# Optimization experiments

Measured on AMD Instinct MI355X. Metric: run time of the kernel, lower is better.

## Reference

```python
import jax, jax.numpy as jnp
import numpy as np

N = 50000       # nodes
E = 800000      # directed edges (before self-loops)
IN_C = 128
HID = 32
HEADS = 4
OUT_C = 64
NEG_SLOPE = 0.2  # PyG GATConv default leaky relu slope


def setup_inputs() -> dict:
    key = jax.random.key(0)
    ks = jax.random.split(key, 11)
    x = jax.random.normal(ks[0], (N, IN_C), jnp.float32)
    edge_index = jax.random.randint(ks[1], (2, E), 0, N, dtype=jnp.int32)
    # conv1: in -> HEADS*HID, concat=True
    W1 = jax.random.normal(ks[2], (IN_C, HEADS * HID), jnp.float32) / np.sqrt(IN_C)
    att_src1 = jax.random.normal(ks[3], (HEADS, HID), jnp.float32) / np.sqrt(HID)
    att_dst1 = jax.random.normal(ks[4], (HEADS, HID), jnp.float32) / np.sqrt(HID)
    b1 = jnp.zeros((HEADS * HID,), jnp.float32)
    # conv2: HEADS*HID -> OUT_C, heads=1, concat=False
    W2 = jax.random.normal(ks[5], (HEADS * HID, OUT_C), jnp.float32) / np.sqrt(HEADS * HID)
    att_src2 = jax.random.normal(ks[6], (1, OUT_C), jnp.float32) / np.sqrt(OUT_C)
    att_dst2 = jax.random.normal(ks[7], (1, OUT_C), jnp.float32) / np.sqrt(OUT_C)
    b2 = jnp.zeros((OUT_C,), jnp.float32)
    return dict(x=x, edge_index=edge_index, W1=W1, att_src1=att_src1,
                att_dst1=att_dst1, b1=b1, W2=W2, att_src2=att_src2,
                att_dst2=att_dst2, b2=b2)


def _gat_conv(x, src, dst, W, att_src, att_dst, bias, heads, ch, concat):
    # x: [N, F_in]; src/dst: [E'] (self-loops already included)
    h = (x @ W).reshape(N, heads, ch)                 # [N, H, C]
    a_s = jnp.sum(h * att_src[None], axis=-1)         # [N, H]
    a_d = jnp.sum(h * att_dst[None], axis=-1)         # [N, H]
    e = jax.nn.leaky_relu(a_s[src] + a_d[dst], NEG_SLOPE)  # [E', H]
    # numerically-stable edge softmax over destination neighborhoods
    m = jax.ops.segment_max(e, dst, num_segments=N)   # [N, H]
    m = jnp.where(jnp.isfinite(m), m, 0.0)
    ee = jnp.exp(e - jax.lax.stop_gradient(m)[dst])
    denom = jax.ops.segment_sum(ee, dst, num_segments=N)  # [N, H]
    alpha = ee / (denom[dst] + 1e-16)                 # [E', H]
    msg = h[src] * alpha[:, :, None]                  # [E', H, C]
    out = jax.ops.segment_sum(msg, dst, num_segments=N)   # [N, H, C]
    if concat:
        out = out.reshape(N, heads * ch)
    else:
        out = out.mean(axis=1)
    return out + bias


def reference(x, edge_index, W1, att_src1, att_dst1, b1, W2, att_src2, att_dst2, b2):
    # PyG GATConv adds self-loops by default
    loop = jnp.arange(N, dtype=edge_index.dtype)
    src = jnp.concatenate([edge_index[0], loop])
    dst = jnp.concatenate([edge_index[1], loop])
    # dropout layers are identity in eval mode (training=False)
    h = _gat_conv(x, src, dst, W1, att_src1, att_dst1, b1, HEADS, HID, True)
    h = jax.nn.elu(h)
    out = _gat_conv(h, src, dst, W2, att_src2, att_dst2, b2, 1, OUT_C, False)
    return out
```

## Files before the change

kernel.cpp:

```cpp
#include <hip/hip_runtime.h>
#include <math.h>

namespace {
constexpr int N_   = 50000;
constexpr int E_   = 800000;
constexpr int EP_  = E_ + N_;
constexpr float SLOPE = 0.2f;

constexpr int NB_    = (N_ + 127) / 128;
constexpr int CHUNK_ = 8192;
constexpr int NBLKA_ = (EP_ + CHUNK_ - 1) / CHUNK_;
constexpr int CAPB_  = 4096;
constexpr int NBLKG_ = (N_ + 63) / 64;

constexpr size_t OFF_H1  = 0;
constexpr size_t OFF_Y1  = OFF_H1  + (size_t)N_ * 128 * 2;
constexpr size_t OFF_H2  = OFF_Y1  + (size_t)N_ * 128 * 2;
constexpr size_t OFF_AS1 = OFF_H2  + (size_t)N_ * 64 * 2;
constexpr size_t OFF_AD1 = OFF_AS1 + (size_t)N_ * 4 * 4;
constexpr size_t OFF_AS2 = OFF_AD1 + (size_t)N_ * 4 * 4;
constexpr size_t OFF_AD2 = OFF_AS2 + (size_t)N_ * 4;
constexpr size_t OFF_ROW = OFF_AD2 + (size_t)N_ * 4;
constexpr size_t OFF_GC  = OFF_ROW + (((size_t)(N_ + 1) * 4 + 15) & ~(size_t)15);
constexpr size_t OFF_GO  = OFF_GC  + (((size_t)NB_ * 4 + 15) & ~(size_t)15);
constexpr size_t OFF_GU  = OFF_GO  + (((size_t)(NB_ + 1) * 4 + 15) & ~(size_t)15);
constexpr size_t OFF_EB1 = OFF_GU  + (((size_t)NB_ * 4 + 15) & ~(size_t)15);
constexpr size_t OFF_EB  = OFF_EB1 + (size_t)EP_ * 4;
}

typedef __attribute__((ext_vector_type(8))) short short8;
typedef __attribute__((ext_vector_type(4))) float f32x4;

__device__ __forceinline__ unsigned short f2bf(float x) {
  unsigned u = __float_as_uint(x);
  return (unsigned short)((u + 0x7FFFu + ((u >> 16) & 1u)) >> 16);
}
__device__ __forceinline__ unsigned pack2bf(float a, float b) {
  return (unsigned)f2bf(a) | ((unsigned)f2bf(b) << 16);
}
__device__ __forceinline__ float bf_lo(unsigned u) { return __uint_as_float(u << 16); }
__device__ __forceinline__ float bf_hi(unsigned u) { return __uint_as_float(u & 0xFFFF0000u); }

__global__ __launch_bounds__(256, 3) void k_gemm1(const float* __restrict__ x,
    const float* __restrict__ W, const float* __restrict__ av_s,
    const float* __restrict__ av_d, unsigned short* __restrict__ hbf,
    float* __restrict__ a_s, float* __restrict__ a_d)
{
  __shared__ __align__(16) char smem[52224];
  unsigned short* xs = (unsigned short*)smem;
  unsigned*       wt = (unsigned*)(smem + 17408);
  float*         wtf = (float*)(smem + 17408);
  const int t = threadIdx.x;
  const int rbase = blockIdx.x * 64;
#pragma unroll
  for (int it = 0; it < 8; ++it) {
    const int fidx = t + it * 256;
    const int row = fidx >> 5;
    const int c4  = fidx & 31;
    const int rg  = rbase + row;
    float4 v = (rg < N_) ? ((const float4*)x)[(size_t)rg * 32 + c4]
                         : make_float4(0.f, 0.f, 0.f, 0.f);
    *(uint2*)&xs[row * 136 + c4 * 4] =
        make_uint2(pack2bf(v.x, v.y), pack2bf(v.z, v.w));
  }
#pragma unroll
  for (int it = 0; it < 32; ++it) {
    const int idx = t + it * 256;
    const int n  = idx & 127;
    const int kk = idx >> 7;
    wt[n * 68 + kk] = pack2bf(W[(2 * kk) * 128 + n], W[(2 * kk + 1) * 128 + n]);
  }
  __syncthreads();
  const int wv = t >> 6;
  const int l  = t & 63;
  const int lr = l & 15;
  const int lg = l >> 4;
  f32x4 acc[8];
#pragma unroll
  for (int j = 0; j < 8; ++j) acc[j] = (f32x4){0.f, 0.f, 0.f, 0.f};
#pragma unroll
  for (int ks = 0; ks < 4; ++ks) {
    const short8 a = *(const short8*)&xs[(wv * 16 + lr) * 136 + ks * 32 + lg * 8];
#pragma unroll
    for (int j = 0; j < 8; ++j) {
      const short8 b = *(const short8*)&wt[(j * 16 + lr) * 68 + ks * 16 + lg * 4];
      acc[j] = __builtin_amdgcn_mfma_f32_16x16x32_bf16(a, b, acc[j], 0, 0, 0);
    }
  }
  __syncthreads();
#pragma unroll
  for (int j = 0; j < 8; ++j)
#pragma unroll
    for (int r = 0; r < 4; ++r)
      wtf[(wv * 16 + lg * 4 + r) * 132 + j * 16 + lr] = acc[j][r];
  __syncthreads();
#pragma unroll
  for (int it = 0; it < 16; ++it) {
    const int idx = t + it * 256;
    const int row = idx >> 6;
    const int c2  = idx & 63;
    const int rg  = rbase + row;
    if (rg < N_) {
      const float2 hv = *(const float2*)&wtf[row * 132 + c2 * 2];
      ((unsigned*)hbf)[(size_t)rg * 64 + c2] = pack2bf(hv.x, hv.y);
    }
  }
  {
    const int row = t & 63;
    const int q   = t >> 6;
    const int rg  = rbase + row;
    float ss = 0.f, sd = 0.f;
#pragma unroll
    for (int i = 0; i < 8; ++i) {
      const float4 hv = *(const float4*)&wtf[row * 132 + q * 32 + 4 * i];
      const float4 s4 = *(const float4*)&av_s[q * 32 + 4 * i];
      const float4 d4 = *(const float4*)&av_d[q * 32 + 4 * i];
      ss += hv.x * s4.x + hv.y * s4.y + hv.z * s4.z + hv.w * s4.w;
      sd += hv.x * d4.x + hv.y * d4.y + hv.z * d4.z + hv.w * d4.w;
    }
    if (rg < N_) { a_s[rg * 4 + q] = ss; a_d[rg * 4 + q] = sd; }
  }
}

__global__ __launch_bounds__(256, 4) void k_gemm2(const unsigned* __restrict__ ybf,
    const float* __restrict__ W, const float* __restrict__ av_s,
    const float* __restrict__ av_d, unsigned short* __restrict__ hbf,
    float* __restrict__ a_s, float* __restrict__ a_d)
{
  __shared__ __align__(16) char smem[36864];
  unsigned short* xs = (unsigned short*)smem;
  unsigned*       wt = (unsigned*)(smem + 17408);
  float*         wtf = (float*)(smem + 17408);
  float*          ps = (float*)(smem + 34816);
  const int t = threadIdx.x;
  const int rbase = blockIdx.x * 64;
#pragma unroll
  for (int it = 0; it < 16; ++it) {
    const int idx = t + it * 256;
    const int row = idx >> 6;
    const int c2  = idx & 63;
    const int rg  = rbase + row;
    const unsigned u = (rg < N_) ? ybf[(size_t)rg * 64 + c2] : 0u;
    *(unsigned*)&xs[row * 136 + c2 * 2] = u;
  }
#pragma unroll
  for (int it = 0; it < 16; ++it) {
    const int idx = t + it * 256;
    const int n  = idx & 63;
    const int kk = idx >> 6;
    wt[n * 68 + kk] = pack2bf(W[(2 * kk) * 64 + n], W[(2 * kk + 1) * 64 + n]);
  }
  __syncthreads();
  const int wv = t >> 6;
  const int l  = t & 63;
  const int lr = l & 15;
  const int lg = l >> 4;
  f32x4 acc[4];
#pragma unroll
  for (int j = 0; j < 4; ++j) acc[j] = (f32x4){0.f, 0.f, 0.f, 0.f};
#pragma unroll
  for (int ks = 0; ks < 4; ++ks) {
    const short8 a = *(const short8*)&xs[(wv * 16 + lr) * 136 + ks * 32 + lg * 8];
#pragma unroll
    for (int j = 0; j < 4; ++j) {
      const short8 b = *(const short8*)&wt[(j * 16 + lr) * 68 + ks * 16 + lg * 4];
      acc[j] = __builtin_amdgcn_mfma_f32_16x16x32_bf16(a, b, acc[j], 0, 0, 0);
    }
  }
  __syncthreads();
#pragma unroll
  for (int j = 0; j < 4; ++j)
#pragma unroll
    for (int r = 0; r < 4; ++r)
      wtf[(wv * 16 + lg * 4 + r) * 68 + j * 16 + lr] = acc[j][r];
  __syncthreads();
#pragma unroll
  for (int it = 0; it < 8; ++it) {
    const int idx = t + it * 256;
    const int row = idx >> 5;
    const int c2  = idx & 31;
    const int rg  = rbase + row;
    if (rg < N_) {
      const float2 hv = *(const float2*)&wtf[row * 68 + c2 * 2];
      ((unsigned*)hbf)[(size_t)rg * 32 + c2] = pack2bf(hv.x, hv.y);
    }
  }
  {
    const int row = t & 63;
    const int g   = t >> 6;
    float ss = 0.f, sd = 0.f;
#pragma unroll
    for (int i = 0; i < 4; ++i) {
      const float4 hv = *(const float4*)&wtf[row * 68 + g * 16 + 4 * i];
      const float4 s4 = *(const float4*)&av_s[g * 16 + 4 * i];
      const float4 d4 = *(const float4*)&av_d[g * 16 + 4 * i];
      ss += hv.x * s4.x + hv.y * s4.y + hv.z * s4.z + hv.w * s4.w;
      sd += hv.x * d4.x + hv.y * d4.y + hv.z * d4.z + hv.w * d4.w;
    }
    ps[g * 64 + row] = ss;
    ps[256 + g * 64 + row] = sd;
  }
  __syncthreads();
  if (t < 64) {
    const int rg = rbase + t;
    if (rg < N_) {
      a_s[rg] = ps[t] + ps[64 + t] + ps[128 + t] + ps[192 + t];
      a_d[rg] = ps[256 + t] + ps[320 + t] + ps[384 + t] + ps[448 + t];
    }
  }
}

__global__ __launch_bounds__(256) void k_hist(const int* __restrict__ ei,
                                              int* __restrict__ gcount)
{
  __shared__ int nh[NB_];
  const int t = threadIdx.x;
  for (int j = t; j < NB_; j += 256) nh[j] = 0;
  __syncthreads();
  const int beg = blockIdx.x * CHUNK_;
  const int end = min(beg + CHUNK_, EP_);
  for (int i = beg + t; i < end; i += 256) {
    const int d = (i < E_) ? ei[E_ + i] : (i - E_);
    atomicAdd(&nh[d >> 7], 1);
  }
  __syncthreads();
  for (int j = t; j < NB_; j += 256)
    if (nh[j]) atomicAdd(&gcount[j], nh[j]);
}

__global__ __launch_bounds__(512) void k_scan(const int* __restrict__ gcount,
    int* __restrict__ goff, int* __restrict__ gcursor)
{
  __shared__ int sd[512];
  const int t = threadIdx.x;
  const int v = (t < NB_) ? gcount[t] : 0;
  sd[t] = v;
  __syncthreads();
  for (int off = 1; off < 512; off <<= 1) {
    const int add = (t >= off) ? sd[t - off] : 0;
    __syncthreads();
    sd[t] += add;
    __syncthreads();
  }
  if (t < NB_) { goff[t] = sd[t] - v; gcursor[t] = sd[t] - v; }
  if (t == 0) goff[NB_] = EP_;
}

__global__ __launch_bounds__(256) void k_scatter(const int* __restrict__ ei,
    int* __restrict__ gcursor, unsigned* __restrict__ eb1)
{
  __shared__ int nh[NB_];
  __shared__ int gb[NB_];
  const int t = threadIdx.x;
  for (int j = t; j < NB_; j += 256) nh[j] = 0;
  __syncthreads();
  const int beg = blockIdx.x * CHUNK_;
  const int end = min(beg + CHUNK_, EP_);
  for (int i = beg + t; i < end; i += 256) {
    const int d = (i < E_) ? ei[E_ + i] : (i - E_);
    atomicAdd(&nh[d >> 7], 1);
  }
  __syncthreads();
  for (int j = t; j < NB_; j += 256) {
    const int c = nh[j];
    gb[j] = c ? atomicAdd(&gcursor[j], c) : 0;
    nh[j] = 0;
  }
  __syncthreads();
  for (int i = beg + t; i < end; i += 256) {
    int s, d;
    if (i < E_) { s = ei[i]; d = ei[E_ + i]; } else { s = d = i - E_; }
    const int b = d >> 7;
    const int r = atomicAdd(&nh[b], 1);
    eb1[gb[b] + r] = ((unsigned)s << 16) | (unsigned)d;
  }
}

__global__ __launch_bounds__(256) void k_bucket(const unsigned* __restrict__ eb1,
    const int* __restrict__ goff, int* __restrict__ rowptr,
    int* __restrict__ ebuf)
{
  __shared__ int h[128];
  __shared__ int off[129];
  __shared__ unsigned arrv[CAPB_];
  const int b = blockIdx.x;
  const int t = threadIdx.x;
  const int base = goff[b];
  const int cnt  = goff[b + 1] - base;
  if (t < 128) h[t] = 0;
  __syncthreads();
  const bool fits = (cnt <= CAPB_);
  for (int i = t; i < cnt; i += 256) {
    const unsigned v = eb1[base + i];
    if (fits) arrv[i] = v;
    atomicAdd(&h[(int)(v & 0xFFFFu) - (b << 7)], 1);
  }
  __syncthreads();
  if (t < 64) {
    const int a0 = h[2 * t], a1 = h[2 * t + 1];
    int s = a0 + a1;
#pragma unroll
    for (int m = 1; m < 64; m <<= 1) {
      const int u = __shfl_up(s, m);
      if (t >= m) s += u;
    }
    off[2 * t + 1] = s - a1;
    off[2 * t]     = s - a1 - a0;
    if (t == 63) off[128] = s;
  }
  __syncthreads();
  if (t < 128) {
    const int dst = (b << 7) + t;
    if (dst < N_) rowptr[dst] = base + off[t];
  }
  if (b == NB_ - 1 && t == 0) rowptr[N_] = EP_;
  if (t < 128) h[t] = 0;
  __syncthreads();
  for (int i = t; i < cnt; i += 256) {
    const unsigned v = fits ? arrv[i] : eb1[base + i];
    const int dlow = (int)(v & 0xFFFFu) - (b << 7);
    const int r = atomicAdd(&h[dlow], 1);
    ebuf[base + off[dlow] + r] = (int)(v >> 16);
  }
}

__global__ __launch_bounds__(256, 4) void k_agg1(const int* __restrict__ rowptr,
    const int* __restrict__ ebuf, const float* __restrict__ a_s,
    const float* __restrict__ a_d, const unsigned short* __restrict__ hbf,
    const float* __restrict__ b1, unsigned* __restrict__ y)
{
  __shared__ uint2 pl[4][4 * 65];
  const int w = threadIdx.x >> 6;
  const int l = threadIdx.x & 63;
  const int d = blockIdx.x * 4 + w;
  const int base = rowptr[d];
  const int deg  = rowptr[d + 1] - base;
  const float4 ad = *(const float4*)&a_d[(size_t)d * 4];
  const int hsel = l >> 4;
  const unsigned l4 = (unsigned)l * 4u;
  float acc0 = 0.f, acc1 = 0.f;
  float r0, r1, r2, r3;

  if (deg <= 64) {
    int   sreg = 0;
    float e0 = -1e30f, e1 = -1e30f, e2 = -1e30f, e3 = -1e30f;
    if (l < deg) {
      sreg = ebuf[base + l];
      const float4 as = *(const float4*)&a_s[(size_t)sreg * 4];
      e0 = as.x + ad.x; e0 = e0 > 0.f ? e0 : SLOPE * e0;
      e1 = as.y + ad.y; e1 = e1 > 0.f ? e1 : SLOPE * e1;
      e2 = as.z + ad.z; e2 = e2 > 0.f ? e2 : SLOPE * e2;
      e3 = as.w + ad.w; e3 = e3 > 0.f ? e3 : SLOPE * e3;
    }
    float mx0 = e0, mx1 = e1, mx2 = e2, mx3 = e3;
#pragma unroll
    for (int m = 32; m >= 1; m >>= 1) {
      mx0 = fmaxf(mx0, __shfl_xor(mx0, m));
      mx1 = fmaxf(mx1, __shfl_xor(mx1, m));
      mx2 = fmaxf(mx2, __shfl_xor(mx2, m));
      mx3 = fmaxf(mx3, __shfl_xor(mx3, m));
    }
    const float p0 = (l < deg) ? __expf(e0 - mx0) : 0.f;
    const float p1 = (l < deg) ? __expf(e1 - mx1) : 0.f;
    const float p2 = (l < deg) ? __expf(e2 - mx2) : 0.f;
    const float p3 = (l < deg) ? __expf(e3 - mx3) : 0.f;
    float sm0 = p0, sm1 = p1, sm2 = p2, sm3 = p3;
#pragma unroll
    for (int m = 32; m >= 1; m >>= 1) {
      sm0 += __shfl_xor(sm0, m);
      sm1 += __shfl_xor(sm1, m);
      sm2 += __shfl_xor(sm2, m);
      sm3 += __shfl_xor(sm3, m);
    }
    r0 = 1.f / (sm0 + 1e-16f);
    r1 = 1.f / (sm1 + 1e-16f);
    r2 = 1.f / (sm2 + 1e-16f);
    r3 = 1.f / (sm3 + 1e-16f);
    {
      const unsigned soff = (unsigned)sreg << 8;
      pl[w][0 * 65 + l] = make_uint2(soff, __float_as_uint(p0));
      pl[w][1 * 65 + l] = make_uint2(soff, __float_as_uint(p1));
      pl[w][2 * 65 + l] = make_uint2(soff, __float_as_uint(p2));
      pl[w][3 * 65 + l] = make_uint2(soff, __float_as_uint(p3));
    }
    const uint2* __restrict__ rp = &pl[w][hsel * 65];
    const int niter = (deg + 7) >> 3;
    int it = 0;
    for (; it + 2 <= niter; it += 2) {
      unsigned uA[8], uB[8];
      float pA[8], pB[8];
#pragma unroll
      for (int u = 0; u < 8; ++u) {
        const uint2 sp = rp[it * 8 + u];
        pA[u] = __uint_as_float(sp.y);
        uA[u] = *(const unsigned*)((const char*)hbf + (sp.x + l4));
      }
#pragma unroll
      for (int u = 0; u < 8; ++u) {
        const uint2 sp = rp[it * 8 + 8 + u];
        pB[u] = __uint_as_float(sp.y);
        uB[u] = *(const unsigned*)((const char*)hbf + (sp.x + l4));
      }
#pragma unroll
      for (int u = 0; u < 8; ++u) {
        acc0 = fmaf(pA[u], bf_lo(uA[u]), acc0);
        acc1 = fmaf(pA[u], bf_hi(uA[u]), acc1);
      }
#pragma unroll
      for (int u = 0; u < 8; ++u) {
        acc0 = fmaf(pB[u], bf_lo(uB[u]), acc0);
        acc1 = fmaf(pB[u], bf_hi(uB[u]), acc1);
      }
    }
    if (it < niter) {
      unsigned uA[8];
      float pA[8];
#pragma unroll
      for (int u = 0; u < 8; ++u) {
        const uint2 sp = rp[it * 8 + u];
        pA[u] = __uint_as_float(sp.y);
        uA[u] = *(const unsigned*)((const char*)hbf + (sp.x + l4));
      }
#pragma unroll
      for (int u = 0; u < 8; ++u) {
        acc0 = fmaf(pA[u], bf_lo(uA[u]), acc0);
        acc1 = fmaf(pA[u], bf_hi(uA[u]), acc1);
      }
    }
  } else {
    float mx0 = -1e30f, mx1 = -1e30f, mx2 = -1e30f, mx3 = -1e30f;
    for (int i = l; i < deg; i += 64) {
      const int s = ebuf[base + i];
      const float4 as = *(const float4*)&a_s[(size_t)s * 4];
      float e0 = as.x + ad.x; e0 = e0 > 0.f ? e0 : SLOPE * e0;
      float e1 = as.y + ad.y; e1 = e1 > 0.f ? e1 : SLOPE * e1;
      float e2 = as.z + ad.z; e2 = e2 > 0.f ? e2 : SLOPE * e2;
      float e3 = as.w + ad.w; e3 = e3 > 0.f ? e3 : SLOPE * e3;
      mx0 = fmaxf(mx0, e0); mx1 = fmaxf(mx1, e1);
      mx2 = fmaxf(mx2, e2); mx3 = fmaxf(mx3, e3);
    }
#pragma unroll
    for (int m = 32; m >= 1; m >>= 1) {
      mx0 = fmaxf(mx0, __shfl_xor(mx0, m));
      mx1 = fmaxf(mx1, __shfl_xor(mx1, m));
      mx2 = fmaxf(mx2, __shfl_xor(mx2, m));
      mx3 = fmaxf(mx3, __shfl_xor(mx3, m));
    }
    float sm0 = 0.f, sm1 = 0.f, sm2 = 0.f, sm3 = 0.f;
    for (int i = l; i < deg; i += 64) {
      const int s = ebuf[base + i];
      const float4 as = *(const float4*)&a_s[(size_t)s * 4];
      float e0 = as.x + ad.x; e0 = e0 > 0.f ? e0 : SLOPE * e0;
      float e1 = as.y + ad.y; e1 = e1 > 0.f ? e1 : SLOPE * e1;
      float e2 = as.z + ad.z; e2 = e2 > 0.f ? e2 : SLOPE * e2;
      float e3 = as.w + ad.w; e3 = e3 > 0.f ? e3 : SLOPE * e3;
      sm0 += __expf(e0 - mx0); sm1 += __expf(e1 - mx1);
      sm2 += __expf(e2 - mx2); sm3 += __expf(e3 - mx3);
    }
#pragma unroll
    for (int m = 32; m >= 1; m >>= 1) {
      sm0 += __shfl_xor(sm0, m);
      sm1 += __shfl_xor(sm1, m);
      sm2 += __shfl_xor(sm2, m);
      sm3 += __shfl_xor(sm3, m);
    }
    r0 = 1.f / (sm0 + 1e-16f);
    r1 = 1.f / (sm1 + 1e-16f);
    r2 = 1.f / (sm2 + 1e-16f);
    r3 = 1.f / (sm3 + 1e-16f);
    const float mxs = hsel == 3 ? mx3 : hsel == 2 ? mx2 : hsel == 1 ? mx1 : mx0;
    for (int i = 0; i < deg; ++i) {
      const int s = ebuf[base + i];
      const float4 as = *(const float4*)&a_s[(size_t)s * 4];
      float e0 = as.x + ad.x; e0 = e0 > 0.f ? e0 : SLOPE * e0;
      float e1 = as.y + ad.y; e1 = e1 > 0.f ? e1 : SLOPE * e1;
      float e2 = as.z + ad.z; e2 = e2 > 0.f ? e2 : SLOPE * e2;
      float e3 = as.w + ad.w; e3 = e3 > 0.f ? e3 : SLOPE * e3;
      const float es = hsel == 3 ? e3 : hsel == 2 ? e2 : hsel == 1 ? e1 : e0;
      const float pa = __expf(es - mxs);
      const unsigned uu = ((const unsigned*)(hbf + (size_t)s * 128))[l];
      acc0 = fmaf(pa, bf_lo(uu), acc0);
      acc1 = fmaf(pa, bf_hi(uu), acc1);
    }
  }
  const float rsel = hsel == 3 ? r3 : hsel == 2 ? r2 : hsel == 1 ? r1 : r0;
  const int c0 = 2 * l;
  const float2 bb = *(const float2*)&b1[c0];
  float o0 = acc0 * rsel + bb.x;
  float o1 = acc1 * rsel + bb.y;
  o0 = o0 > 0.f ? o0 : expm1f(o0);
  o1 = o1 > 0.f ? o1 : expm1f(o1);
  y[(size_t)d * 64 + l] = pack2bf(o0, o1);
}

__global__ __launch_bounds__(256, 4) void k_agg2(const int* __restrict__ rowptr,
    const int* __restrict__ ebuf, const float* __restrict__ a_s,
    const float* __restrict__ a_d, const unsigned short* __restrict__ hbf,
    const float* __restrict__ b2, float* __restrict__ out)
{
  __shared__ uint2 pl2[4][66];
  const int w = threadIdx.x >> 6;
  const int l = threadIdx.x & 63;
  const int lh = l & 31;
  const bool hi = (l >= 32);
  const int d = blockIdx.x * 4 + w;
  const int base = rowptr[d];
  const int deg  = rowptr[d + 1] - base;
  const float ad = a_d[d];
  const unsigned lh4 = (unsigned)lh * 4u;
  float acc0 = 0.f, acc1 = 0.f;
  float rv;

  if (deg <= 64) {
    int   sreg = 0;
    float e = -1e30f;
    if (l < deg) {
      sreg = ebuf[base + l];
      e = a_s[sreg] + ad; e = e > 0.f ? e : SLOPE * e;
    }
    float mx = e;
#pragma unroll
    for (int m = 32; m >= 1; m >>= 1) mx = fmaxf(mx, __shfl_xor(mx, m));
    const float p = (l < deg) ? __expf(e - mx) : 0.f;
    float sm = p;
#pragma unroll
    for (int m = 32; m >= 1; m >>= 1) sm += __shfl_xor(sm, m);
    rv = 1.f / (sm + 1e-16f);
    pl2[w][l] = make_uint2((unsigned)(l < deg ? sreg : 0) << 7,
                           __float_as_uint(p));
    const uint2* __restrict__ rp = &pl2[w][hi ? 1 : 0];
    const int niter = (deg + 15) >> 4;
    int it = 0;
    for (; it + 2 <= niter; it += 2) {
      unsigned uA[8], uB[8];
      float pA[8], pB[8];
#pragma unroll
      for (int u = 0; u < 8; ++u) {
        const uint2 sp = rp[it * 16 + 2 * u];
        pA[u] = __uint_as_float(sp.y);
        uA[u] = *(const unsigned*)((const char*)hbf + (sp.x + lh4));
      }
#pragma unroll
      for (int u = 0; u < 8; ++u) {
        const uint2 sp = rp[it * 16 + 16 + 2 * u];
        pB[u] = __uint_as_float(sp.y);
        uB[u] = *(const unsigned*)((const char*)hbf + (sp.x + lh4));
      }
#pragma unroll
      for (int u = 0; u < 8; ++u) {
        acc0 = fmaf(pA[u], bf_lo(uA[u]), acc0);
        acc1 = fmaf(pA[u], bf_hi(uA[u]), acc1);
      }
#pragma unroll
      for (int u = 0; u < 8; ++u) {
        acc0 = fmaf(pB[u], bf_lo(uB[u]), acc0);
        acc1 = fmaf(pB[u], bf_hi(uB[u]), acc1);
      }
    }
    if (it < niter) {
      unsigned uA[8];
      float pA[8];
#pragma unroll
      for (int u = 0; u < 8; ++u) {
        const uint2 sp = rp[it * 16 + 2 * u];
        pA[u] = __uint_as_float(sp.y);
        uA[u] = *(const unsigned*)((const char*)hbf + (sp.x + lh4));
      }
#pragma unroll
      for (int u = 0; u < 8; ++u) {
        acc0 = fmaf(pA[u], bf_lo(uA[u]), acc0);
        acc1 = fmaf(pA[u], bf_hi(uA[u]), acc1);
      }
    }
  } else {
    float mx = -1e30f;
    for (int i = l; i < deg; i += 64) {
      const int s = ebuf[base + i];
      float e = a_s[s] + ad; e = e > 0.f ? e : SLOPE * e;
      mx = fmaxf(mx, e);
    }
#pragma unroll
    for (int m = 32; m >= 1; m >>= 1) mx = fmaxf(mx, __shfl_xor(mx, m));
    float sm = 0.f;
    for (int i = l; i < deg; i += 64) {
      const int s = ebuf[base + i];
      float e = a_s[s] + ad; e = e > 0.f ? e : SLOPE * e;
      sm += __expf(e - mx);
    }
#pragma unroll
    for (int m = 32; m >= 1; m >>= 1) sm += __shfl_xor(sm, m);
    rv = 1.f / (sm + 1e-16f);
    for (int i = 0; i < deg; ++i) {
      const int s = ebuf[base + i];
      float e = a_s[s] + ad; e = e > 0.f ? e : SLOPE * e;
      const float pp = hi ? 0.f : __expf(e - mx);
      const unsigned uu = ((const unsigned*)(hbf + (size_t)s * 64))[lh];
      acc0 = fmaf(pp, bf_lo(uu), acc0);
      acc1 = fmaf(pp, bf_hi(uu), acc1);
    }
  }
  acc0 += __shfl_xor(acc0, 32);
  acc1 += __shfl_xor(acc1, 32);
  if (!hi) {
    const int c0 = 2 * lh;
    const float2 bb = *(const float2*)&b2[c0];
    *(float2*)&out[(size_t)d * 64 + c0] =
        make_float2(acc0 * rv + bb.x, acc1 * rv + bb.y);
  }
}

extern "C" void kernel_launch(void* const* d_in, const int* in_sizes, int n_in,
                              void* d_out, int out_size, void* d_ws, size_t ws_size,
                              hipStream_t stream) {
  const float* x     = (const float*)d_in[0];
  const int*   ei    = (const int*)d_in[1];
  const float* W1    = (const float*)d_in[2];
  const float* as1v  = (const float*)d_in[3];
  const float* ad1v  = (const float*)d_in[4];
  const float* b1    = (const float*)d_in[5];
  const float* W2    = (const float*)d_in[6];
  const float* as2v  = (const float*)d_in[7];
  const float* ad2v  = (const float*)d_in[8];
  const float* b2    = (const float*)d_in[9];
  float* out = (float*)d_out;

  char* ws = (char*)d_ws;
  unsigned short* h1 = (unsigned short*)(ws + OFF_H1);
  unsigned* y1       = (unsigned*)(ws + OFF_Y1);
  unsigned short* h2 = (unsigned short*)(ws + OFF_H2);
  float* a_s1 = (float*)(ws + OFF_AS1);
  float* a_d1 = (float*)(ws + OFF_AD1);
  float* a_s2 = (float*)(ws + OFF_AS2);
  float* a_d2 = (float*)(ws + OFF_AD2);
  int* rowptr = (int*)(ws + OFF_ROW);
  int* gcount = (int*)(ws + OFF_GC);
  int* goff   = (int*)(ws + OFF_GO);
  int* gcur   = (int*)(ws + OFF_GU);
  unsigned* eb1 = (unsigned*)(ws + OFF_EB1);
  int* ebuf   = (int*)(ws + OFF_EB);

  hipMemsetAsync(gcount, 0, (size_t)NB_ * 4, stream);

  k_gemm1<<<NBLKG_, 256, 0, stream>>>(x, W1, as1v, ad1v, h1, a_s1, a_d1);
  k_hist<<<NBLKA_, 256, 0, stream>>>(ei, gcount);
  k_scan<<<1, 512, 0, stream>>>(gcount, goff, gcur);
  k_scatter<<<NBLKA_, 256, 0, stream>>>(ei, gcur, eb1);
  k_bucket<<<NB_, 256, 0, stream>>>(eb1, goff, rowptr, ebuf);
  k_agg1<<<N_ / 4, 256, 0, stream>>>(rowptr, ebuf, a_s1, a_d1, h1, b1, y1);
  k_gemm2<<<NBLKG_, 256, 0, stream>>>(y1, W2, as2v, ad2v, h2, a_s2, a_d2);
  k_agg2<<<N_ / 4, 256, 0, stream>>>(rowptr, ebuf, a_s2, a_d2, h2, b2, out);
}
```

Measured before the change: 149.8 us.

## Split agg1 nodes across two waves and fold histogram into gemm1 launch

The layer-1 aggregation now assigns two waves to each destination node. Each wave covers half of the channels, and the two half-waves of a wave process alternating edges; the partial sums are combined with a cross-half shuffle. This shortens the serial edge loop per wave and doubles the grid size. In exchange, the edge-softmax statistics are computed redundantly by both waves. Separately, the degree-histogram kernel is merged into the gemm1 launch as extra blocks, removing one launch and letting the two run concurrently.

After: 178.9 us. +19.4%, slower.

```diff
diff --git a/kernel.cpp b/kernel.cpp
--- a/kernel.cpp
+++ b/kernel.cpp
@@ -41,16 +41,32 @@
 __device__ __forceinline__ float bf_lo(unsigned u) { return __uint_as_float(u << 16); }
 __device__ __forceinline__ float bf_hi(unsigned u) { return __uint_as_float(u & 0xFFFF0000u); }
 
-__global__ __launch_bounds__(256, 3) void k_gemm1(const float* __restrict__ x,
+__global__ __launch_bounds__(256, 3) void k_g1h(const float* __restrict__ x,
     const float* __restrict__ W, const float* __restrict__ av_s,
     const float* __restrict__ av_d, unsigned short* __restrict__ hbf,
-    float* __restrict__ a_s, float* __restrict__ a_d)
+    float* __restrict__ a_s, float* __restrict__ a_d,
+    const int* __restrict__ ei, int* __restrict__ gcount)
 {
   __shared__ __align__(16) char smem[52224];
+  const int t = threadIdx.x;
+  if (blockIdx.x >= NBLKG_) {
+    int* nh = (int*)smem;
+    for (int j = t; j < NB_; j += 256) nh[j] = 0;
+    __syncthreads();
+    const int beg = (blockIdx.x - NBLKG_) * CHUNK_;
+    const int end = min(beg + CHUNK_, EP_);
+    for (int i = beg + t; i < end; i += 256) {
+      const int dd = (i < E_) ? ei[E_ + i] : (i - E_);
+      atomicAdd(&nh[dd >> 7], 1);
+    }
+    __syncthreads();
+    for (int j = t; j < NB_; j += 256)
+      if (nh[j]) atomicAdd(&gcount[j], nh[j]);
+    return;
+  }
   unsigned short* xs = (unsigned short*)smem;
   unsigned*       wt = (unsigned*)(smem + 17408);
   float*         wtf = (float*)(smem + 17408);
-  const int t = threadIdx.x;
   const int rbase = blockIdx.x * 64;
 #pragma unroll
   for (int it = 0; it < 8; ++it) {
@@ -210,24 +226,6 @@
   }
 }
 
-__global__ __launch_bounds__(256) void k_hist(const int* __restrict__ ei,
-                                              int* __restrict__ gcount)
-{
-  __shared__ int nh[NB_];
-  const int t = threadIdx.x;
-  for (int j = t; j < NB_; j += 256) nh[j] = 0;
-  __syncthreads();
-  const int beg = blockIdx.x * CHUNK_;
-  const int end = min(beg + CHUNK_, EP_);
-  for (int i = beg + t; i < end; i += 256) {
-    const int d = (i < E_) ? ei[E_ + i] : (i - E_);
-    atomicAdd(&nh[d >> 7], 1);
-  }
-  __syncthreads();
-  for (int j = t; j < NB_; j += 256)
-    if (nh[j]) atomicAdd(&gcount[j], nh[j]);
-}
-
 __global__ __launch_bounds__(512) void k_scan(const int* __restrict__ gcount,
     int* __restrict__ goff, int* __restrict__ gcursor)
 {
@@ -332,12 +330,15 @@
   __shared__ uint2 pl[4][4 * 65];
   const int w = threadIdx.x >> 6;
   const int l = threadIdx.x & 63;
-  const int d = blockIdx.x * 4 + w;
+  const int d = blockIdx.x * 2 + (w >> 1);
+  const int half = w & 1;
   const int base = rowptr[d];
   const int deg  = rowptr[d + 1] - base;
   const float4 ad = *(const float4*)&a_d[(size_t)d * 4];
-  const int hsel = l >> 4;
-  const unsigned l4 = (unsigned)l * 4u;
+  const int pe = l >> 5;
+  const int ci = half * 32 + (l & 31);
+  const int hsel = ci >> 4;
+  const unsigned ci4 = (unsigned)ci * 4u;
   float acc0 = 0.f, acc1 = 0.f;
   float r0, r1, r2, r3;
 
@@ -383,23 +384,23 @@
       pl[w][2 * 65 + l] = make_uint2(soff, __float_as_uint(p2));
       pl[w][3 * 65 + l] = make_uint2(soff, __float_as_uint(p3));
     }
-    const uint2* __restrict__ rp = &pl[w][hsel * 65];
-    const int niter = (deg + 7) >> 3;
+    const uint2* __restrict__ rp = &pl[w][hsel * 65 + pe];
+    const int niter = (deg + 15) >> 4;
     int it = 0;
     for (; it + 2 <= niter; it += 2) {
       unsigned uA[8], uB[8];
       float pA[8], pB[8];
 #pragma unroll
       for (int u = 0; u < 8; ++u) {
-        const uint2 sp = rp[it * 8 + u];
+        const uint2 sp = rp[it * 16 + 2 * u];
         pA[u] = __uint_as_float(sp.y);
-        uA[u] = *(const unsigned*)((const char*)hbf + (sp.x + l4));
-      }
-#pragma unroll
-      for (int u = 0; u < 8; ++u) {
-        const uint2 sp = rp[it * 8 + 8 + u];
+        uA[u] = *(const unsigned*)((const char*)hbf + (sp.x + ci4));
+      }
+#pragma unroll
+      for (int u = 0; u < 8; ++u) {
+        const uint2 sp = rp[it * 16 + 16 + 2 * u];
         pB[u] = __uint_as_float(sp.y);
-        uB[u] = *(const unsigned*)((const char*)hbf + (sp.x + l4));
+        uB[u] = *(const unsigned*)((const char*)hbf + (sp.x + ci4));
       }
 #pragma unroll
       for (int u = 0; u < 8; ++u) {
@@ -417,9 +418,9 @@
       float pA[8];
 #pragma unroll
       for (int u = 0; u < 8; ++u) {
-        const uint2 sp = rp[it * 8 + u];
+        const uint2 sp = rp[it * 16 + 2 * u];
         pA[u] = __uint_as_float(sp.y);
-        uA[u] = *(const unsigned*)((const char*)hbf + (sp.x + l4));
+        uA[u] = *(const unsigned*)((const char*)hbf + (sp.x + ci4));
       }
 #pragma unroll
       for (int u = 0; u < 8; ++u) {
@@ -469,28 +470,35 @@
     r2 = 1.f / (sm2 + 1e-16f);
     r3 = 1.f / (sm3 + 1e-16f);
     const float mxs = hsel == 3 ? mx3 : hsel == 2 ? mx2 : hsel == 1 ? mx1 : mx0;
-    for (int i = 0; i < deg; ++i) {
-      const int s = ebuf[base + i];
-      const float4 as = *(const float4*)&a_s[(size_t)s * 4];
-      float e0 = as.x + ad.x; e0 = e0 > 0.f ? e0 : SLOPE * e0;
-      float e1 = as.y + ad.y; e1 = e1 > 0.f ? e1 : SLOPE * e1;
-      float e2 = as.z + ad.z; e2 = e2 > 0.f ? e2 : SLOPE * e2;
-      float e3 = as.w + ad.w; e3 = e3 > 0.f ? e3 : SLOPE * e3;
-      const float es = hsel == 3 ? e3 : hsel == 2 ? e2 : hsel == 1 ? e1 : e0;
-      const float pa = __expf(es - mxs);
-      const unsigned uu = ((const unsigned*)(hbf + (size_t)s * 128))[l];
-      acc0 = fmaf(pa, bf_lo(uu), acc0);
-      acc1 = fmaf(pa, bf_hi(uu), acc1);
-    }
-  }
-  const float rsel = hsel == 3 ? r3 : hsel == 2 ? r2 : hsel == 1 ? r1 : r0;
-  const int c0 = 2 * l;
-  const float2 bb = *(const float2*)&b1[c0];
-  float o0 = acc0 * rsel + bb.x;
-  float o1 = acc1 * rsel + bb.y;
-  o0 = o0 > 0.f ? o0 : expm1f(o0);
-  o1 = o1 > 0.f ? o1 : expm1f(o1);
-  y[(size_t)d * 64 + l] = pack2bf(o0, o1);
+    for (int i = 0; i < deg; i += 2) {
+      const int e = i + pe;
+      if (e < deg) {
+        const int s = ebuf[base + e];
+        const float4 as = *(const float4*)&a_s[(size_t)s * 4];
+        float e0 = as.x + ad.x; e0 = e0 > 0.f ? e0 : SLOPE * e0;
+        float e1 = as.y + ad.y; e1 = e1 > 0.f ? e1 : SLOPE * e1;
+        float e2 = as.z + ad.z; e2 = e2 > 0.f ? e2 : SLOPE * e2;
+        float e3 = as.w + ad.w; e3 = e3 > 0.f ? e3 : SLOPE * e3;
+        const float es = hsel == 3 ? e3 : hsel == 2 ? e2 : hsel == 1 ? e1 : e0;
+        const float pa = __expf(es - mxs);
+        const unsigned uu = ((const unsigned*)(hbf + (size_t)s * 128))[ci];
+        acc0 = fmaf(pa, bf_lo(uu), acc0);
+        acc1 = fmaf(pa, bf_hi(uu), acc1);
+      }
+    }
+  }
+  acc0 += __shfl_xor(acc0, 32);
+  acc1 += __shfl_xor(acc1, 32);
+  if (pe == 0) {
+    const float rsel = hsel == 3 ? r3 : hsel == 2 ? r2 : hsel == 1 ? r1 : r0;
+    const int c0 = 2 * ci;
+    const float2 bb = *(const float2*)&b1[c0];
+    float o0 = acc0 * rsel + bb.x;
+    float o1 = acc1 * rsel + bb.y;
+    o0 = o0 > 0.f ? o0 : expm1f(o0);
+    o1 = o1 > 0.f ? o1 : expm1f(o1);
+    y[(size_t)d * 64 + ci] = pack2bf(o0, o1);
+  }
 }
 
 __global__ __launch_bounds__(256, 4) void k_agg2(const int* __restrict__ rowptr,
@@ -641,12 +649,12 @@
 
   hipMemsetAsync(gcount, 0, (size_t)NB_ * 4, stream);
 
-  k_gemm1<<<NBLKG_, 256, 0, stream>>>(x, W1, as1v, ad1v, h1, a_s1, a_d1);
-  k_hist<<<NBLKA_, 256, 0, stream>>>(ei, gcount);
+  k_g1h<<<NBLKG_ + NBLKA_, 256, 0, stream>>>(x, W1, as1v, ad1v, h1, a_s1, a_d1,
+                                             ei, gcount);
   k_scan<<<1, 512, 0, stream>>>(gcount, goff, gcur);
   k_scatter<<<NBLKA_, 256, 0, stream>>>(ei, gcur, eb1);
   k_bucket<<<NB_, 256, 0, stream>>>(eb1, goff, rowptr, ebuf);
-  k_agg1<<<N_ / 4, 256, 0, stream>>>(rowptr, ebuf, a_s1, a_d1, h1, b1, y1);
+  k_agg1<<<N_ / 2, 256, 0, stream>>>(rowptr, ebuf, a_s1, a_d1, h1, b1, y1);
   k_gemm2<<<NBLKG_, 256, 0, stream>>>(y1, W2, as2v, ad2v, h2, a_s2, a_d2);
   k_agg2<<<N_ / 4, 256, 0, stream>>>(rowptr, ebuf, a_s2, a_d2, h2, b2, out);
 }
```

## Fuse histogram into gemm1 launch and sort agg1 edges by source chunk

Applied to the files above, without the earlier changes.

The destination histogram kernel is merged into the first GEMM kernel as extra blocks, removing one launch and letting the histogram run alongside the GEMM. In the layer-1 aggregation, each wave sorts its edge list in shared memory by a coarse source-index bucket (sreg>>13) using ballots and popcounts, so that gathers of h rows from nearby sources are grouped for better cache locality. This adds eight ballots and some ALU work per node. The GEMM blocks now share their launch with lighter histogram blocks.

Measured after the change: 147.7 us. About the same (-1.4%).

```diff
diff --git a/kernel.cpp b/kernel.cpp
--- a/kernel.cpp
+++ b/kernel.cpp
@@ -41,16 +41,32 @@
 __device__ __forceinline__ float bf_lo(unsigned u) { return __uint_as_float(u << 16); }
 __device__ __forceinline__ float bf_hi(unsigned u) { return __uint_as_float(u & 0xFFFF0000u); }
 
-__global__ __launch_bounds__(256, 3) void k_gemm1(const float* __restrict__ x,
+__global__ __launch_bounds__(256, 3) void k_g1h(const float* __restrict__ x,
     const float* __restrict__ W, const float* __restrict__ av_s,
     const float* __restrict__ av_d, unsigned short* __restrict__ hbf,
-    float* __restrict__ a_s, float* __restrict__ a_d)
+    float* __restrict__ a_s, float* __restrict__ a_d,
+    const int* __restrict__ ei, int* __restrict__ gcount)
 {
   __shared__ __align__(16) char smem[52224];
+  const int t = threadIdx.x;
+  if (blockIdx.x >= NBLKG_) {
+    int* nh = (int*)smem;
+    for (int j = t; j < NB_; j += 256) nh[j] = 0;
+    __syncthreads();
+    const int beg = (blockIdx.x - NBLKG_) * CHUNK_;
+    const int end = min(beg + CHUNK_, EP_);
+    for (int i = beg + t; i < end; i += 256) {
+      const int dd = (i < E_) ? ei[E_ + i] : (i - E_);
+      atomicAdd(&nh[dd >> 7], 1);
+    }
+    __syncthreads();
+    for (int j = t; j < NB_; j += 256)
+      if (nh[j]) atomicAdd(&gcount[j], nh[j]);
+    return;
+  }
   unsigned short* xs = (unsigned short*)smem;
   unsigned*       wt = (unsigned*)(smem + 17408);
   float*         wtf = (float*)(smem + 17408);
-  const int t = threadIdx.x;
   const int rbase = blockIdx.x * 64;
 #pragma unroll
   for (int it = 0; it < 8; ++it) {
@@ -208,24 +224,6 @@
       a_d[rg] = ps[256 + t] + ps[320 + t] + ps[384 + t] + ps[448 + t];
     }
   }
-}
-
-__global__ __launch_bounds__(256) void k_hist(const int* __restrict__ ei,
-                                              int* __restrict__ gcount)
-{
-  __shared__ int nh[NB_];
-  const int t = threadIdx.x;
-  for (int j = t; j < NB_; j += 256) nh[j] = 0;
-  __syncthreads();
-  const int beg = blockIdx.x * CHUNK_;
-  const int end = min(beg + CHUNK_, EP_);
-  for (int i = beg + t; i < end; i += 256) {
-    const int d = (i < E_) ? ei[E_ + i] : (i - E_);
-    atomicAdd(&nh[d >> 7], 1);
-  }
-  __syncthreads();
-  for (int j = t; j < NB_; j += 256)
-    if (nh[j]) atomicAdd(&gcount[j], nh[j]);
 }
 
 __global__ __launch_bounds__(512) void k_scan(const int* __restrict__ gcount,
@@ -376,12 +374,38 @@
     r1 = 1.f / (sm1 + 1e-16f);
     r2 = 1.f / (sm2 + 1e-16f);
     r3 = 1.f / (sm3 + 1e-16f);
+    const int cc = (l < deg) ? (sreg >> 13) : 7;
+    const unsigned long long lt = (l == 0) ? 0ull : (~0ull >> (64 - l));
+    const unsigned long long c0b = __ballot(cc == 0);
+    const unsigned long long c1b = __ballot(cc == 1);
+    const unsigned long long c2b = __ballot(cc == 2);
+    const unsigned long long c3b = __ballot(cc == 3);
+    const unsigned long long c4b = __ballot(cc == 4);
+    const unsigned long long c5b = __ballot(cc == 5);
+    const unsigned long long c6b = __ballot(cc == 6);
+    const unsigned long long c7b = __ballot(cc == 7);
+    unsigned long long bsel = c0b;
+    bsel = (cc == 1) ? c1b : bsel;
+    bsel = (cc == 2) ? c2b : bsel;
+    bsel = (cc == 3) ? c3b : bsel;
+    bsel = (cc == 4) ? c4b : bsel;
+    bsel = (cc == 5) ? c5b : bsel;
+    bsel = (cc == 6) ? c6b : bsel;
+    bsel = (cc == 7) ? c7b : bsel;
+    int pos = __popcll(bsel & lt);
+    pos += (cc > 0) ? __popcll(c0b) : 0;
+    pos += (cc > 1) ? __popcll(c1b) : 0;
+    pos += (cc > 2) ? __popcll(c2b) : 0;
+    pos += (cc > 3) ? __popcll(c3b) : 0;
+    pos += (cc > 4) ? __popcll(c4b) : 0;
+    pos += (cc > 5) ? __popcll(c5b) : 0;
+    pos += (cc > 6) ? __popcll(c6b) : 0;
     {
       const unsigned soff = (unsigned)sreg << 8;
-      pl[w][0 * 65 + l] = make_uint2(soff, __float_as_uint(p0));
-      pl[w][1 * 65 + l] = make_uint2(soff, __float_as_uint(p1));
-      pl[w][2 * 65 + l] = make_uint2(soff, __float_as_uint(p2));
-      pl[w][3 * 65 + l] = make_uint2(soff, __float_as_uint(p3));
+      pl[w][0 * 65 + pos] = make_uint2(soff, __float_as_uint(p0));
+      pl[w][1 * 65 + pos] = make_uint2(soff, __float_as_uint(p1));
+      pl[w][2 * 65 + pos] = make_uint2(soff, __float_as_uint(p2));
+      pl[w][3 * 65 + pos] = make_uint2(soff, __float_as_uint(p3));
     }
     const uint2* __restrict__ rp = &pl[w][hsel * 65];
     const int niter = (deg + 7) >> 3;
@@ -641,8 +665,8 @@
 
   hipMemsetAsync(gcount, 0, (size_t)NB_ * 4, stream);
 
-  k_gemm1<<<NBLKG_, 256, 0, stream>>>(x, W1, as1v, ad1v, h1, a_s1, a_d1);
-  k_hist<<<NBLKA_, 256, 0, stream>>>(ei, gcount);
+  k_g1h<<<NBLKG_ + NBLKA_, 256, 0, stream>>>(x, W1, as1v, ad1v, h1, a_s1, a_d1,
+                                             ei, gcount);
   k_scan<<<1, 512, 0, stream>>>(gcount, goff, gcur);
   k_scatter<<<NBLKA_, 256, 0, stream>>>(ei, gcur, eb1);
   k_bucket<<<NB_, 256, 0, stream>>>(eb1, goff, rowptr, ebuf);
```
